# Kernel optimization log

Measured on AMD Instinct MI355X. Metric: run time of the kernel, lower is better.

The kernel has to match this reference:

```python
import jax, jax.numpy as jnp
import numpy as np

LENGTH = 14
THRESHOLD = 0.6
R = 5


def setup_inputs() -> dict:
    key = jax.random.key(0)
    B = 131072
    heatmap = jax.random.uniform(key, (B, 1, LENGTH, LENGTH), dtype=jnp.float32)
    return {"heatmap": heatmap}


def _nms_masks(heatmap):
    hm = heatmap[:, 0]  # [B,14,14]
    B = hm.shape[0]
    heat = jnp.where(hm > THRESHOLD, hm, 0.0).reshape(B, LENGTH * LENGTH)
    grid = jnp.arange(LENGTH)
    idxs = []
    # 4 rounds of argmax + zero-out-window suppression (fixed small loop)
    for _ in range(4):
        idx = jnp.argmax(heat, axis=1)  # [B]
        x = idx // LENGTH
        y = idx % LENGTH
        x1 = jnp.maximum(x - R, 0)
        y1 = jnp.maximum(y - R, 0)
        x2 = jnp.minimum(x + R, 15)  # original clamps at 15 (exclusive end)
        y2 = jnp.minimum(y + R, 15)
        rowm = (grid[None, :] >= x1[:, None]) & (grid[None, :] < x2[:, None])  # [B,14]
        colm = (grid[None, :] >= y1[:, None]) & (grid[None, :] < y2[:, None])  # [B,14]
        win = (rowm[:, :, None] & colm[:, None, :]).reshape(B, LENGTH * LENGTH)
        heat = jnp.where(win, 0.0, heat)
        idxs.append(idx)
    idxs = jnp.stack(idxs, axis=1)  # [B,4]
    coords = jnp.stack([idxs // LENGTH, idxs % LENGTH], axis=-1)  # [B,4,2]
    # pickTwo: choose the pair (among the 6) with max squared distance
    pairs = jnp.array([[0, 1], [0, 2], [0, 3], [1, 2], [1, 3], [2, 3]])
    pc = coords[:, pairs]  # [B,6,2,2]
    dists = jnp.sum((pc[:, :, 1] - pc[:, :, 0]) ** 2, axis=-1)  # [B,6]
    best = jnp.argmax(dists, axis=1)  # [B] (first max on ties, like np.argmax)
    co = jnp.take_along_axis(pc, best[:, None, None, None], axis=1)[:, 0]  # [B,2,2]
    # Voronoi-style masks: pixel belongs to mask1 iff strictly closer to co1
    u = jnp.arange(LENGTH)[:, None]  # [14,1]
    v = jnp.arange(LENGTH)[None, :]  # [1,14]
    d1 = (u[None] - co[:, 0, 0, None, None]) ** 2 + (v[None] - co[:, 0, 1, None, None]) ** 2
    d2 = (u[None] - co[:, 1, 0, None, None]) ** 2 + (v[None] - co[:, 1, 1, None, None]) ** 2
    m1 = (d1 < d2).astype(jnp.float32)  # [B,14,14]
    m2 = 1.0 - m1  # (m1 < 0.9).float() with m1 in {0,1}
    return m1[:, None], m2[:, None]  # [B,1,14,14] each


def reference(heatmap):
    return _nms_masks(heatmap)
```

## Files before the change

kernel.cpp:

```cpp
#include <hip/hip_runtime.h>


constexpr int L = 14;
constexpr int NPIX = L * L;
constexpr int NV4 = NPIX / 4;

__global__ __launch_bounds__(256) void nms_kernel(const float4* __restrict__ hm4,
                                                  float4* __restrict__ out4,
                                                  int B) {
    const int lane = threadIdx.x & 63;
    const int b = (blockIdx.x << 2) + (threadIdx.x >> 6);
    if (b >= B) return;

    const bool act = (lane < NV4);

    float4 v4;
    if (act) v4 = hm4[(size_t)b * NV4 + lane];
    else     v4 = make_float4(-1.f, -1.f, -1.f, -1.f);

    float va[4] = {v4.x, v4.y, v4.z, v4.w};
    if (act) {
#pragma unroll
        for (int e = 0; e < 4; ++e) va[e] = (va[e] > 0.6f) ? va[e] : 0.0f;
    }

    int xs[4], ys[4];
#pragma unroll
    for (int e = 0; e < 4; ++e) {
        const int flat = 4 * lane + e;
        xs[e] = act ? (flat / L) : 1000;
        ys[e] = act ? (flat % L) : 1000;
    }

    int idxs[4];
#pragma unroll
    for (int r = 0; r < 4; ++r) {
        float mv = fmaxf(fmaxf(va[0], va[1]), fmaxf(va[2], va[3]));
#pragma unroll
        for (int off = 1; off < 64; off <<= 1)
            mv = fmaxf(mv, __shfl_xor(mv, off, 64));

        const bool h0 = (va[0] == mv), h1 = (va[1] == mv),
                   h2 = (va[2] == mv), h3 = (va[3] == mv);
        int e_loc = h0 ? 0 : (h1 ? 1 : (h2 ? 2 : 3));
        const unsigned long long ball = __ballot(h0 | h1 | h2 | h3);
        const int fl = __ffsll(ball) - 1;
        const int e0 = __shfl(e_loc, fl, 64);
        const int idx = 4 * fl + e0;
        idxs[r] = idx;

        if (r < 3) {
            const int ax = idx / L, ay = idx % L;
            const int wx1 = max(ax - 5, 0), wx2 = min(ax + 5, 15);
            const int wy1 = max(ay - 5, 0), wy2 = min(ay + 5, 15);
#pragma unroll
            for (int e = 0; e < 4; ++e) {
                const bool in = (xs[e] >= wx1) & (xs[e] < wx2) &
                                (ys[e] >= wy1) & (ys[e] < wy2);
                va[e] = in ? 0.0f : va[e];
            }
        }
    }

    int cx[4], cy[4];
#pragma unroll
    for (int i = 0; i < 4; ++i) { cx[i] = idxs[i] / L; cy[i] = idxs[i] % L; }

    const int pa[6] = {0, 0, 0, 1, 1, 2};
    const int pb[6] = {1, 2, 3, 2, 3, 3};
    int bestd = -1, bi = 0;
#pragma unroll
    for (int p = 0; p < 6; ++p) {
        const int dx = cx[pb[p]] - cx[pa[p]];
        const int dy = cy[pb[p]] - cy[pa[p]];
        const int d = dx * dx + dy * dy;
        if (d > bestd) { bestd = d; bi = p; }
    }
    const int ax0 = cx[pa[bi]], ay0 = cy[pa[bi]];
    const int ax1 = cx[pb[bi]], ay1 = cy[pb[bi]];

    float m1[4], m2[4];
#pragma unroll
    for (int e = 0; e < 4; ++e) {
        const int du1 = xs[e] - ax0, dv1 = ys[e] - ay0;
        const int du2 = xs[e] - ax1, dv2 = ys[e] - ay1;
        const int d1 = du1 * du1 + dv1 * dv1;
        const int d2 = du2 * du2 + dv2 * dv2;
        m1[e] = (d1 < d2) ? 1.0f : 0.0f;
        m2[e] = 1.0f - m1[e];
    }

    if (act) {
        out4[(size_t)b * NV4 + lane] = make_float4(m1[0], m1[1], m1[2], m1[3]);
        out4[(size_t)(B + b) * NV4 + lane] = make_float4(m2[0], m2[1], m2[2], m2[3]);
    }
}

extern "C" void kernel_launch(void* const* d_in, const int* in_sizes, int n_in,
                              void* d_out, int out_size, void* d_ws, size_t ws_size,
                              hipStream_t stream) {
    const float4* hm4 = (const float4*)d_in[0];
    float4* out4 = (float4*)d_out;
    const int B = in_sizes[0] / NPIX;
    const int blocks = (B + 3) / 4;
    nms_kernel<<<blocks, 256, 0, stream>>>(hm4, out4, B);
}
```

Measured before the change: 296.8 us.

## Map one heatmap per 16-lane row and reduce with DPP row ops

Each wavefront now handles four heatmaps, one per 16-lane DPP row, and each lane holds up to 16 pixels. The old design used one 64-lane wave per heatmap with only 49 lanes active. The cross-lane argmax now uses in-row DPP max/min reductions in place of a full-wave shuffle butterfly plus ballot and shuffle. The goal is to cut idle lanes and the latency of cross-lane communication, at the cost of more registers and serial per-lane work. Memory accesses stay float4 but become strided within each row.

```diff
diff --git a/kernel.cpp b/kernel.cpp
--- a/kernel.cpp
+++ b/kernel.cpp
@@ -5,66 +5,90 @@
 constexpr int NPIX = L * L;
 constexpr int NV4 = NPIX / 4;
 
+template <int CTRL>
+__device__ __forceinline__ float dpp_maxf(float x) {
+    int y = __builtin_amdgcn_update_dpp(0, __float_as_int(x), CTRL, 0xF, 0xF, true);
+    return fmaxf(x, __int_as_float(y));
+}
+template <int CTRL>
+__device__ __forceinline__ int dpp_mini(int x) {
+    int y = __builtin_amdgcn_update_dpp(0, x, CTRL, 0xF, 0xF, true);
+    return min(x, y);
+}
+__device__ __forceinline__ float row_max16(float x) {
+    x = dpp_maxf<0xB1>(x);
+    x = dpp_maxf<0x4E>(x);
+    x = dpp_maxf<0x141>(x);
+    x = dpp_maxf<0x140>(x);
+    return x;
+}
+__device__ __forceinline__ int row_min16(int x) {
+    x = dpp_mini<0xB1>(x);
+    x = dpp_mini<0x4E>(x);
+    x = dpp_mini<0x141>(x);
+    x = dpp_mini<0x140>(x);
+    return x;
+}
+
 __global__ __launch_bounds__(256) void nms_kernel(const float4* __restrict__ hm4,
                                                   float4* __restrict__ out4,
                                                   int B) {
     const int lane = threadIdx.x & 63;
-    const int b = (blockIdx.x << 2) + (threadIdx.x >> 6);
+    const int s = lane & 15;
+    const int b = blockIdx.x * 16 + ((threadIdx.x >> 6) << 2) + (lane >> 4);
     if (b >= B) return;
 
-    const bool act = (lane < NV4);
+    const float4* __restrict__ bp = hm4 + (size_t)b * NV4;
 
-    float4 v4;
-    if (act) v4 = hm4[(size_t)b * NV4 + lane];
-    else     v4 = make_float4(-1.f, -1.f, -1.f, -1.f);
+    float4 a0 = bp[s];
+    float4 a1 = bp[16 + s];
+    float4 a2 = bp[32 + s];
+    float4 a3 = (s == 0) ? bp[48] : make_float4(-1.f, -1.f, -1.f, -1.f);
 
-    float va[4] = {v4.x, v4.y, v4.z, v4.w};
-    if (act) {
+    float va[16] = {a0.x, a0.y, a0.z, a0.w, a1.x, a1.y, a1.z, a1.w,
+                    a2.x, a2.y, a2.z, a2.w, a3.x, a3.y, a3.z, a3.w};
+
+    const int s4 = s << 2;
+    int fl[16], px[16];
 #pragma unroll
-        for (int e = 0; e < 4; ++e) va[e] = (va[e] > 0.6f) ? va[e] : 0.0f;
-    }
-
-    int xs[4], ys[4];
-#pragma unroll
-    for (int e = 0; e < 4; ++e) {
-        const int flat = 4 * lane + e;
-        xs[e] = act ? (flat / L) : 1000;
-        ys[e] = act ? (flat % L) : 1000;
+    for (int i = 0; i < 16; ++i) {
+        const bool real = (i < 12) || (s == 0);
+        fl[i] = s4 + ((i >> 2) << 6) + (i & 3);
+        const int x = fl[i] / L, y = fl[i] - x * L;
+        px[i] = real ? ((x << 5) | y) : ((31 << 5) | 31);
+        va[i] = (va[i] > 0.6f) ? va[i] : (real ? 0.0f : -1.0f);
     }
 
     int idxs[4];
 #pragma unroll
     for (int r = 0; r < 4; ++r) {
-        float mv = fmaxf(fmaxf(va[0], va[1]), fmaxf(va[2], va[3]));
+        float mv = va[0];
 #pragma unroll
-        for (int off = 1; off < 64; off <<= 1)
-            mv = fmaxf(mv, __shfl_xor(mv, off, 64));
+        for (int i = 1; i < 16; ++i) mv = fmaxf(mv, va[i]);
+        mv = row_max16(mv);
 
-        const bool h0 = (va[0] == mv), h1 = (va[1] == mv),
-                   h2 = (va[2] == mv), h3 = (va[3] == mv);
-        int e_loc = h0 ? 0 : (h1 ? 1 : (h2 ? 2 : 3));
-        const unsigned long long ball = __ballot(h0 | h1 | h2 | h3);
-        const int fl = __ffsll(ball) - 1;
-        const int e0 = __shfl(e_loc, fl, 64);
-        const int idx = 4 * fl + e0;
+        int fc = 1 << 20;
+#pragma unroll
+        for (int i = 15; i >= 0; --i) fc = (va[i] == mv) ? fl[i] : fc;
+        const int idx = row_min16(fc);
         idxs[r] = idx;
 
         if (r < 3) {
-            const int ax = idx / L, ay = idx % L;
+            const int ax = idx / L, ay = idx - (idx / L) * L;
             const int wx1 = max(ax - 5, 0), wx2 = min(ax + 5, 15);
             const int wy1 = max(ay - 5, 0), wy2 = min(ay + 5, 15);
 #pragma unroll
-            for (int e = 0; e < 4; ++e) {
-                const bool in = (xs[e] >= wx1) & (xs[e] < wx2) &
-                                (ys[e] >= wy1) & (ys[e] < wy2);
-                va[e] = in ? 0.0f : va[e];
+            for (int i = 0; i < 16; ++i) {
+                const int x = px[i] >> 5, y = px[i] & 31;
+                const bool in = (x >= wx1) & (x < wx2) & (y >= wy1) & (y < wy2);
+                va[i] = in ? 0.0f : va[i];
             }
         }
     }
 
     int cx[4], cy[4];
 #pragma unroll
-    for (int i = 0; i < 4; ++i) { cx[i] = idxs[i] / L; cy[i] = idxs[i] % L; }
+    for (int i = 0; i < 4; ++i) { cx[i] = idxs[i] / L; cy[i] = idxs[i] - (idxs[i] / L) * L; }
 
     const int pa[6] = {0, 0, 0, 1, 1, 2};
     const int pb[6] = {1, 2, 3, 2, 3, 3};
@@ -79,20 +103,26 @@
     const int ax0 = cx[pa[bi]], ay0 = cy[pa[bi]];
     const int ax1 = cx[pb[bi]], ay1 = cy[pb[bi]];
 
-    float m1[4], m2[4];
+    float m[16];
 #pragma unroll
-    for (int e = 0; e < 4; ++e) {
-        const int du1 = xs[e] - ax0, dv1 = ys[e] - ay0;
-        const int du2 = xs[e] - ax1, dv2 = ys[e] - ay1;
-        const int d1 = du1 * du1 + dv1 * dv1;
-        const int d2 = du2 * du2 + dv2 * dv2;
-        m1[e] = (d1 < d2) ? 1.0f : 0.0f;
-        m2[e] = 1.0f - m1[e];
+    for (int i = 0; i < 16; ++i) {
+        const int x = px[i] >> 5, y = px[i] & 31;
+        const int du1 = x - ax0, dv1 = y - ay0;
+        const int du2 = x - ax1, dv2 = y - ay1;
+        m[i] = ((du1 * du1 + dv1 * dv1) < (du2 * du2 + dv2 * dv2)) ? 1.0f : 0.0f;
     }
 
-    if (act) {
-        out4[(size_t)b * NV4 + lane] = make_float4(m1[0], m1[1], m1[2], m1[3]);
-        out4[(size_t)(B + b) * NV4 + lane] = make_float4(m2[0], m2[1], m2[2], m2[3]);
+    float4* __restrict__ o1 = out4 + (size_t)b * NV4;
+    float4* __restrict__ o2 = out4 + (size_t)(B + b) * NV4;
+    o1[s]      = make_float4(m[0], m[1], m[2], m[3]);
+    o1[16 + s] = make_float4(m[4], m[5], m[6], m[7]);
+    o1[32 + s] = make_float4(m[8], m[9], m[10], m[11]);
+    o2[s]      = make_float4(1.f - m[0], 1.f - m[1], 1.f - m[2], 1.f - m[3]);
+    o2[16 + s] = make_float4(1.f - m[4], 1.f - m[5], 1.f - m[6], 1.f - m[7]);
+    o2[32 + s] = make_float4(1.f - m[8], 1.f - m[9], 1.f - m[10], 1.f - m[11]);
+    if (s == 0) {
+        o1[48] = make_float4(m[12], m[13], m[14], m[15]);
+        o2[48] = make_float4(1.f - m[12], 1.f - m[13], 1.f - m[14], 1.f - m[15]);
     }
 }
 
@@ -102,6 +132,6 @@
     const float4* hm4 = (const float4*)d_in[0];
     float4* out4 = (float4*)d_out;
     const int B = in_sizes[0] / NPIX;
-    const int blocks = (B + 3) / 4;
+    const int blocks = (B + 15) / 16;
     nms_kernel<<<blocks, 256, 0, stream>>>(hm4, out4, B);
 }
```

New measurement: 279.6 us. 5.8% less time.
